# Optimization experiments

Measured on AMD Instinct MI355X. Metric: run time of the kernel, lower is better.

The kernel has to match this reference:

```python
import jax, jax.numpy as jnp
import numpy as np

EPS = 1e-8      # covariance regularizer (module-level `eps` in source repo)
ALPHA = 0.8     # style/content blend (module-level `alpha` in source repo)
SV_THRESH = 1e-5  # singular-value cutoff from the source


def _flatten(x):
    # x: [1, H, W, C] -> [C, H*W]
    xt = jnp.transpose(x[0], (2, 0, 1))  # C, H, W
    C = xt.shape[0]
    return xt.reshape(C, -1)


def _cov(f):
    # f: [C, N] already centered -> [C, C]
    C, N = f.shape
    return f @ f.T / (jnp.float32(N) - 1.0) + EPS * jnp.eye(C, dtype=f.dtype)


def _masked_pow(S, p):
    # Faithful to truncating columns with S <= 1e-5: zero their diag weight.
    mask = S > SV_THRESH
    S_safe = jnp.where(mask, S, 1.0)
    return jnp.where(mask, S_safe ** p, 0.0)


def setup_inputs() -> dict:
    key = jax.random.key(0)
    k1, k2 = jax.random.split(key)
    content = jax.random.normal(k1, (1, 128, 128, 512), dtype=jnp.float32)
    style = jax.random.normal(k2, (1, 128, 128, 512), dtype=jnp.float32)
    return {"content": content, "style": style}


def reference(content, style):
    H, W, C = content.shape[1], content.shape[2], content.shape[3]

    content_flat = _flatten(content)  # [C, Hc*Wc]
    style_flat = _flatten(style)      # [C, Hs*Ws]

    mc = content_flat.mean(axis=1, keepdims=True)
    fc = content_flat - mc
    ms = style_flat.mean(axis=1, keepdims=True)
    fs = style_flat - ms

    fcfc = _cov(fc)
    fsfs = _cov(fs)

    # tf.svd on a symmetric PSD matrix: S descending, U orthonormal.
    Uc, Sc, _ = jnp.linalg.svd(fcfc)
    Us, Ss, _ = jnp.linalg.svd(fsfs)

    # Whitening: Uc diag(Sc^-1/2) Uc^T (truncated cols == zeroed diag entries)
    Dc = _masked_pow(Sc, -0.5)
    whiten = (Uc * Dc[None, :]) @ Uc.T  # [C, C]
    fc_hat = whiten @ fc                # [C, N]

    # Coloring: Us diag(Ss^1/2) Us^T
    Ds = _masked_pow(Ss, 0.5)
    color = (Us * Ds[None, :]) @ Us.T
    fcs_hat = color @ fc_hat + ms

    blended = ALPHA * fcs_hat + (1.0 - ALPHA) * (fc + mc)  # [C, N]
    blended = blended.reshape(C, H, W)
    return jnp.transpose(blended, (1, 2, 0))[None]  # [1, H, W, C]
```

## Files before the change

### kernel.cpp

```cpp
#include <hip/hip_runtime.h>
#include <math.h>

#define NPIX 16384
#define CCH  512
#define MS   262144

typedef unsigned short u16;
typedef unsigned int u32;
typedef __attribute__((ext_vector_type(8))) short bf16x8;
typedef __attribute__((ext_vector_type(4))) float f32x4;

__device__ __forceinline__ u16 f2bf(float f) {
  u32 u = __builtin_bit_cast(u32, f);
  u += 0x7fffu + ((u >> 16) & 1u);
  return (u16)(u >> 16);
}
__device__ __forceinline__ float b2f(u16 h) {
  u32 u = ((u32)h) << 16;
  return __builtin_bit_cast(float, u);
}

typedef const __attribute__((address_space(1))) u32* gp_t;
typedef __attribute__((address_space(3))) u32* lp_t;
__device__ __forceinline__ void gl_lds16(const void* g, void* l) {
  __builtin_amdgcn_global_load_lds((gp_t)g, (lp_t)l, 16, 0, 0);
}

__device__ __forceinline__ void stage4(const u16* tile, size_t stride, int rl,
                                       int k0, u16* lds, int lane) {
  int lr = lane >> 4;
  int cg = (lane & 15) ^ ((rl + lr) & 15);
  gl_lds16(tile + (size_t)(rl + lr) * stride + k0 + cg * 8,
           lds + (size_t)rl * 128);
}
__device__ __forceinline__ bf16x8 fragld(const u16* lds, int row, int cl) {
  return *(const bf16x8*)&lds[(size_t)row * 128 + (size_t)((cl ^ (row & 15)) << 3)];
}

__device__ __forceinline__ void stage8_64(const u16* tile, size_t stride, int rl,
                                          int k0, u16* lds, int lane) {
  int lr = lane >> 3;
  int cg = (lane & 7) ^ ((rl + lr) & 7);
  gl_lds16(tile + (size_t)(rl + lr) * stride + k0 + cg * 8,
           lds + (size_t)rl * 64);
}
__device__ __forceinline__ bf16x8 fragld64(const u16* lds, int row, int cl) {
  return *(const bf16x8*)&lds[(size_t)row * 64 + (size_t)((cl ^ (row & 7)) << 3)];
}

__global__ __launch_bounds__(256) void prep_k(const float* __restrict__ Xc,
                                              const float* __restrict__ Xs,
                                              float* __restrict__ sums,
                                              u16* __restrict__ fct,
                                              u16* __restrict__ fcb) {
  int b = blockIdx.z;
  const float* X = b ? Xs : Xc;
  u16* outT = fct + (size_t)b * ((size_t)CCH * NPIX);
  __shared__ float T[64][65];
  __shared__ float red2[64][4];
  int n0 = blockIdx.x * 64, c0 = blockIdx.y * 64;
  int t = threadIdx.x;
  int cr = t & 15, nr = t >> 4;
  #pragma unroll
  for (int rr = 0; rr < 4; ++rr) {
    int n = nr + rr * 16;
    float4 v = *(const float4*)&X[(size_t)(n0 + n) * CCH + c0 + cr * 4];
    T[n][cr * 4 + 0] = v.x;
    T[n][cr * 4 + 1] = v.y;
    T[n][cr * 4 + 2] = v.z;
    T[n][cr * 4 + 3] = v.w;
    if (b == 0) {
      ushort4 q;
      q.x = f2bf(v.x); q.y = f2bf(v.y); q.z = f2bf(v.z); q.w = f2bf(v.w);
      *(ushort4*)&fcb[(size_t)(n0 + n) * CCH + c0 + cr * 4] = q;
    }
  }
  __syncthreads();
  int cl = t >> 2, np = (t & 3) * 16;
  size_t obase = (size_t)(c0 + cl) * NPIX + n0 + np;
  float s = 0.f;
  #pragma unroll
  for (int i = 0; i < 16; i += 4) {
    float v0 = T[np + i + 0][cl], v1 = T[np + i + 1][cl];
    float v2 = T[np + i + 2][cl], v3 = T[np + i + 3][cl];
    s += v0 + v1 + v2 + v3;
    ushort4 o;
    o.x = f2bf(v0); o.y = f2bf(v1); o.z = f2bf(v2); o.w = f2bf(v3);
    *(ushort4*)&outT[obase + i] = o;
  }
  red2[cl][t & 3] = s;
  __syncthreads();
  if (t < 64) {
    float cs = red2[t][0] + red2[t][1] + red2[t][2] + red2[t][3];
    atomicAdd(&sums[b * CCH + c0 + t], cs);
  }
}

__global__ __launch_bounds__(256, 4) void gram_mfma(const u16* __restrict__ fct,
                                                    float* __restrict__ G) {
  int kc = blockIdx.x;
  int pair = blockIdx.y;
  int b = blockIdx.z;
  int bi = pair >> 2, bj = pair & 3;
  const u16* Xb = fct + (size_t)b * ((size_t)CCH * NPIX);
  float* Gb = G + (size_t)b * MS;
  __shared__ u16 As[128 * 64];
  __shared__ u16 Bs[128 * 64];
  int tid = threadIdx.x, w = tid >> 6, lane = tid & 63;
  int qm = w & 1, qn = w >> 1;
  const u16* ssrc = (w < 2) ? Xb + (size_t)(bi * 128) * NPIX
                            : Xb + (size_t)(bj * 128) * NPIX;
  u16* sdst = (w < 2) ? As : Bs;
  int rbase = (w & 1) * 64;
  f32x4 acc[4][4];
  #pragma unroll
  for (int t = 0; t < 4; ++t)
    #pragma unroll
    for (int u = 0; u < 4; ++u) acc[t][u] = (f32x4)(0.f);

  for (int st = 0; st < 8; ++st) {
    int k0 = kc * 512 + st * 64;
    __syncthreads();
    #pragma unroll
    for (int i = 0; i < 8; ++i) stage8_64(ssrc, NPIX, rbase + i * 8, k0, sdst, lane);
    __syncthreads();
    #pragma unroll
    for (int s = 0; s < 2; ++s) {
      int cl = s * 4 + (lane >> 4);
      bf16x8 a[4], bb[4];
      #pragma unroll
      for (int t = 0; t < 4; ++t) a[t] = fragld64(As, qm * 64 + t * 16 + (lane & 15), cl);
      #pragma unroll
      for (int u = 0; u < 4; ++u) bb[u] = fragld64(Bs, qn * 64 + u * 16 + (lane & 15), cl);
      #pragma unroll
      for (int t = 0; t < 4; ++t)
        #pragma unroll
        for (int u = 0; u < 4; ++u)
          acc[t][u] = __builtin_amdgcn_mfma_f32_16x16x32_bf16(a[t], bb[u], acc[t][u], 0, 0, 0);
    }
  }
  #pragma unroll
  for (int t = 0; t < 4; ++t) {
    int row0 = bi * 128 + qm * 64 + t * 16 + (lane >> 4) * 4;
    #pragma unroll
    for (int u = 0; u < 4; ++u) {
      int col = bj * 128 + qn * 64 + u * 16 + (lane & 15);
      #pragma unroll
      for (int r4 = 0; r4 < 4; ++r4)
        atomicAdd(&Gb[(size_t)(row0 + r4) * CCH + col], acc[t][u][r4]);
    }
  }
}

__global__ __launch_bounds__(256) void cov_k(const float* __restrict__ G,
                                             const float* __restrict__ sums,
                                             float* __restrict__ cov,
                                             float* __restrict__ rowsum) {
  int idx = blockIdx.x * 256 + threadIdx.x;
  int b = idx >> 18;
  int ij = idx & (MS - 1);
  int i = ij >> 9, j = ij & 511;
  const float* s = sums + b * CCH;
  float v = (G[idx] - s[i] * s[j] * (1.f / (float)NPIX)) * (1.f / (float)(NPIX - 1));
  if (i == j) v += 1e-8f;
  cov[idx] = v;
  __shared__ float red[256];
  int t = threadIdx.x;
  red[t] = fabsf(v);
  __syncthreads();
  for (int st = 128; st > 0; st >>= 1) {
    if (t < st) red[t] += red[t + st];
    __syncthreads();
  }
  if (t == 0) atomicAdd(&rowsum[b * CCH + i], red[0]);
}

__global__ __launch_bounds__(256) void nsinit_k(const float* __restrict__ cov,
                                                const float* __restrict__ rowsum,
                                                float* __restrict__ snorm,
                                                float* __restrict__ coef,
                                                u16* __restrict__ Anh,
                                                u16* __restrict__ Anl,
                                                u16* __restrict__ Z0) {
  __shared__ float red[256];
  int tid = threadIdx.x, blk = blockIdx.x;
  float m = fmaxf(rowsum[tid], rowsum[tid + 256]);
  red[tid] = m; __syncthreads();
  for (int s = 128; s > 0; s >>= 1) {
    if (tid < s) red[tid] = fmaxf(red[tid], red[tid + s]);
    __syncthreads();
  }
  float snc = red[0]; __syncthreads();
  m = fmaxf(rowsum[512 + tid], rowsum[768 + tid]);
  red[tid] = m; __syncthreads();
  for (int s = 128; s > 0; s >>= 1) {
    if (tid < s) red[tid] = fmaxf(red[tid], red[tid + s]);
    __syncthreads();
  }
  float sns = red[0];
  if (blk == 0 && tid == 0) {
    snorm[0] = snc; snorm[1] = sns;
    coef[0] = 0.8f * sqrtf(sns / snc);
  }
  int idx = blk * 256 + tid;
  int b = idx >> 18;
  int ij = idx & (MS - 1);
  int diag = (ij >> 9) == (ij & 511);
  float av = cov[idx] * (b ? 1.f / sns : 1.f / snc);
  u16 hi = f2bf(av);
  Anh[idx] = hi;
  Anl[idx] = f2bf(av - b2f(hi));
  float t0 = (diag ? 3.f - av : -av) * 0.70710678f;
  Z0[idx] = f2bf(t0);
}

struct MM16 {
  const u16* A[4];
  const u16* B[4];
  void* D[4];
  float scale, diag;
  int outFp32;
};

__global__ __launch_bounds__(256) void mm16_k(MM16 args) {
  int z = blockIdx.z;
  const u16* __restrict__ A = args.A[z];
  const u16* __restrict__ B = args.B[z];
  int bi = blockIdx.y, bj = blockIdx.x;
  __shared__ u16 As[64 * 128];
  __shared__ u16 Bs[64 * 128];
  int tid = threadIdx.x, w = tid >> 6, lane = tid & 63;
  int qm = w & 1, qn = w >> 1;
  const u16* ssrc = ((w < 2) ? A + (size_t)(bi * 64) * CCH : B + (size_t)(bj * 64) * CCH);
  u16* sdst = (w < 2) ? As : Bs;
  int rbase = (w & 1) * 32;
  f32x4 acc[2][2];
  #pragma unroll
  for (int t = 0; t < 2; ++t)
    #pragma unroll
    for (int u = 0; u < 2; ++u) acc[t][u] = (f32x4)(0.f);

  for (int st = 0; st < 4; ++st) {
    int k0 = st * 128;
    __syncthreads();
    #pragma unroll
    for (int i = 0; i < 8; ++i) stage4(ssrc, CCH, rbase + i * 4, k0, sdst, lane);
    __syncthreads();
    #pragma unroll
    for (int s = 0; s < 4; ++s) {
      int cl = s * 4 + (lane >> 4);
      bf16x8 a[2], bb[2];
      #pragma unroll
      for (int t = 0; t < 2; ++t) a[t] = fragld(As, qm * 32 + t * 16 + (lane & 15), cl);
      #pragma unroll
      for (int u = 0; u < 2; ++u) bb[u] = fragld(Bs, qn * 32 + u * 16 + (lane & 15), cl);
      #pragma unroll
      for (int t = 0; t < 2; ++t)
        #pragma unroll
        for (int u = 0; u < 2; ++u)
          acc[t][u] = __builtin_amdgcn_mfma_f32_16x16x32_bf16(a[t], bb[u], acc[t][u], 0, 0, 0);
    }
  }
  float sc = args.scale;
  #pragma unroll
  for (int t = 0; t < 2; ++t) {
    int row0 = bi * 64 + qm * 32 + t * 16 + (lane >> 4) * 4;
    #pragma unroll
    for (int u = 0; u < 2; ++u) {
      int col = bj * 64 + qn * 32 + u * 16 + (lane & 15);
      #pragma unroll
      for (int r4 = 0; r4 < 4; ++r4) {
        float v = sc * acc[t][u][r4];
        if (row0 + r4 == col) v += args.diag;
        size_t o = (size_t)(row0 + r4) * CCH + col;
        if (args.outFp32) ((float*)args.D[z])[o] = v;
        else ((u16*)args.D[z])[o] = f2bf(v);
      }
    }
  }
}

__global__ __launch_bounds__(256) void symsplit_k(const float* __restrict__ src,
                                                  u16* __restrict__ hi,
                                                  u16* __restrict__ lo) {
  int b = blockIdx.y;
  int ij = blockIdx.x * 256 + threadIdx.x;
  int i = ij >> 9, j = ij & 511;
  size_t base = (size_t)b * MS;
  float v = 0.5f * (src[base + ij] + src[base + (size_t)j * CCH + i]);
  u16 h = f2bf(v);
  hi[base + ij] = h;
  lo[base + ij] = f2bf(v - b2f(h));
}

struct MMS {
  const u16 *Ah[4], *Al[4], *Bh[4], *Bl[4];
  const u16 *Eh[4], *El[4];
  u16 *Dh[4], *Dl[4];
  float *D32[4];
  u16 *Db[4];
  float scale, beta;
  const float* coefPtr;
};

__global__ __launch_bounds__(256) void mmsplit_k(MMS args) {
  int z = blockIdx.z;
  int bi = blockIdx.y, bj = blockIdx.x;
  __shared__ u16 Ash[64 * 128], Asl[64 * 128], Bsh[64 * 128], Bsl[64 * 128];
  int tid = threadIdx.x, w = tid >> 6, lane = tid & 63;
  int qm = w & 1, qn = w >> 1;
  const u16* sp = (w == 0) ? args.Ah[z] : (w == 1) ? args.Al[z]
                : (w == 2) ? args.Bh[z] : args.Bl[z];
  const u16* ssrc = sp + (size_t)(((w < 2) ? bi : bj) * 64) * CCH;
  u16* sdst = (w == 0) ? Ash : (w == 1) ? Asl : (w == 2) ? Bsh : Bsl;
  f32x4 acc[2][2];
  #pragma unroll
  for (int t = 0; t < 2; ++t)
    #pragma unroll
    for (int u = 0; u < 2; ++u) acc[t][u] = (f32x4)(0.f);

  for (int st = 0; st < 4; ++st) {
    int k0 = st * 128;
    __syncthreads();
    #pragma unroll
    for (int i = 0; i < 16; ++i) stage4(ssrc, CCH, i * 4, k0, sdst, lane);
    __syncthreads();
    #pragma unroll
    for (int s = 0; s < 4; ++s) {
      int cl = s * 4 + (lane >> 4);
      bf16x8 ah[2], al[2], bh[2], bl[2];
      #pragma unroll
      for (int t = 0; t < 2; ++t) {
        int row = qm * 32 + t * 16 + (lane & 15);
        ah[t] = fragld(Ash, row, cl);
        al[t] = fragld(Asl, row, cl);
      }
      #pragma unroll
      for (int u = 0; u < 2; ++u) {
        int row = qn * 32 + u * 16 + (lane & 15);
        bh[u] = fragld(Bsh, row, cl);
        bl[u] = fragld(Bsl, row, cl);
      }
      #pragma unroll
      for (int t = 0; t < 2; ++t)
        #pragma unroll
        for (int u = 0; u < 2; ++u) {
          acc[t][u] = __builtin_amdgcn_mfma_f32_16x16x32_bf16(ah[t], bh[u], acc[t][u], 0, 0, 0);
          acc[t][u] = __builtin_amdgcn_mfma_f32_16x16x32_bf16(ah[t], bl[u], acc[t][u], 0, 0, 0);
          acc[t][u] = __builtin_amdgcn_mfma_f32_16x16x32_bf16(al[t], bh[u], acc[t][u], 0, 0, 0);
        }
    }
  }
  float sc = args.scale;
  if (args.coefPtr) sc *= *args.coefPtr;
  #pragma unroll
  for (int t = 0; t < 2; ++t) {
    int row0 = bi * 64 + qm * 32 + t * 16 + (lane >> 4) * 4;
    #pragma unroll
    for (int u = 0; u < 2; ++u) {
      int col = bj * 64 + qn * 32 + u * 16 + (lane & 15);
      #pragma unroll
      for (int r4 = 0; r4 < 4; ++r4) {
        size_t o = (size_t)(row0 + r4) * CCH + col;
        float v = sc * acc[t][u][r4];
        if (args.beta != 0.f) v += args.beta * (b2f(args.Eh[z][o]) + b2f(args.El[z][o]));
        if (args.D32[z]) args.D32[z][o] = v;
        if (args.Dh[z]) {
          u16 h = f2bf(v);
          args.Dh[z][o] = h;
          args.Dl[z][o] = f2bf(v - b2f(h));
        }
        if (args.Db[z]) args.Db[z][o] = f2bf(v);
      }
    }
  }
}

__global__ __launch_bounds__(256) void mconst_k(const u16* __restrict__ Mb,
                                                const float* __restrict__ sums,
                                                float* __restrict__ mconst) {
  int c = blockIdx.x * 8 + (threadIdx.x >> 5);
  int l = threadIdx.x & 31;
  float s = 0.f;
  #pragma unroll
  for (int k = 0; k < 16; ++k) {
    int j = l + 32 * k;
    s += b2f(Mb[(size_t)c * CCH + j]) * sums[j];
  }
  s += __shfl_down(s, 16, 32);
  s += __shfl_down(s, 8, 32);
  s += __shfl_down(s, 4, 32);
  s += __shfl_down(s, 2, 32);
  s += __shfl_down(s, 1, 32);
  if (l == 0) mconst[c] = (0.8f * sums[512 + c] - s) * (1.f / (float)NPIX);
}

__global__ __launch_bounds__(256) void apply_mfma(const u16* __restrict__ fcb,
                                                  const u16* __restrict__ Mb,
                                                  const float* __restrict__ mconst,
                                                  const float* __restrict__ X,
                                                  float* __restrict__ out) {
  int bi = blockIdx.y;
  int bj = blockIdx.x;
  __shared__ u16 As[128 * 128];
  __shared__ u16 Bs[128 * 128];
  int tid = threadIdx.x, w = tid >> 6, lane = tid & 63;
  int qm = w & 1, qn = w >> 1;
  const u16* ssrc = (w < 2) ? fcb + (size_t)(bi * 128) * CCH
                            : Mb + (size_t)(bj * 128) * CCH;
  u16* sdst = (w < 2) ? As : Bs;
  int rbase = (w & 1) * 64;
  f32x4 acc[4][4];
  #pragma unroll
  for (int t = 0; t < 4; ++t)
    #pragma unroll
    for (int u = 0; u < 4; ++u) acc[t][u] = (f32x4)(0.f);

  for (int st = 0; st < 4; ++st) {
    int k0 = st * 128;
    __syncthreads();
    #pragma unroll
    for (int i = 0; i < 16; ++i) stage4(ssrc, CCH, rbase + i * 4, k0, sdst, lane);
    __syncthreads();
    #pragma unroll
    for (int s = 0; s < 4; ++s) {
      int cl = s * 4 + (lane >> 4);
      bf16x8 a[4], bb[4];
      #pragma unroll
      for (int t = 0; t < 4; ++t) a[t] = fragld(As, qm * 64 + t * 16 + (lane & 15), cl);
      #pragma unroll
      for (int u = 0; u < 4; ++u) bb[u] = fragld(Bs, qn * 64 + u * 16 + (lane & 15), cl);
      #pragma unroll
      for (int t = 0; t < 4; ++t)
        #pragma unroll
        for (int u = 0; u < 4; ++u)
          acc[t][u] = __builtin_amdgcn_mfma_f32_16x16x32_bf16(a[t], bb[u], acc[t][u], 0, 0, 0);
    }
  }
  #pragma unroll
  for (int t = 0; t < 4; ++t) {
    int row0 = bi * 128 + qm * 64 + t * 16 + (lane >> 4) * 4;
    #pragma unroll
    for (int u = 0; u < 4; ++u) {
      int col = bj * 128 + qn * 64 + u * 16 + (lane & 15);
      float cst = mconst[col];
      #pragma unroll
      for (int r4 = 0; r4 < 4; ++r4) {
        size_t o = (size_t)(row0 + r4) * CCH + col;
        out[o] = acc[t][u][r4] + cst + 0.2f * X[o];
      }
    }
  }
}

extern "C" void kernel_launch(void* const* d_in, const int* in_sizes, int n_in,
                              void* d_out, int out_size, void* d_ws, size_t ws_size,
                              hipStream_t stream) {
  const float* Xc = (const float*)d_in[0];
  const float* Xs = (const float*)d_in[1];
  float* out = (float*)d_out;

  float* f = (float*)d_ws;
  float* sums   = f;
  float* rowsum = f + 1024;
  float* G      = f + 2048;
  float* cov    = G + 2 * MS;
  float* snorm  = cov + 2 * MS;
  float* coef   = snorm + 8;
  float* mconst = coef + 8;
  float* Zf     = mconst + 512;

  u16* h   = (u16*)(Zf + 2 * MS);
  u16* fct = h;
  u16* fcb = h + (size_t)2 * CCH * NPIX;
  const size_t B2 = 2 * MS;
  u16* Anh  = fct + 0 * B2;
  u16* Anl  = fct + 1 * B2;
  u16* Y1   = fct + 2 * B2;
  u16* Ya   = fct + 3 * B2;
  u16* Z0   = fct + 4 * B2;
  u16* Z1   = fct + 5 * B2;
  u16* Tb   = fct + 6 * B2;
  u16* Zfsh = fct + 7 * B2;
  u16* Zfsl = fct + 8 * B2;
  u16* Ph   = fct + 9 * B2;
  u16* Pl   = fct + 10 * B2;
  u16* Qh   = fct + 11 * B2;
  u16* Ql   = fct + 12 * B2;
  u16* Zrsh = fct + 13 * B2;
  u16* Zrsl = fct + 14 * B2;
  u16* W2h  = fct + 15 * B2;
  u16* W2l  = W2h + MS;
  u16* Mb   = W2l + MS;

  hipMemsetAsync(d_ws, 0, (2048 + 2 * MS) * sizeof(float), stream);

  prep_k<<<dim3(256, 8, 2), 256, 0, stream>>>(Xc, Xs, sums, fct, fcb);
  gram_mfma<<<dim3(32, 16, 2), 256, 0, stream>>>(fct, G);
  cov_k<<<2048, 256, 0, stream>>>(G, sums, cov, rowsum);
  nsinit_k<<<2048, 256, 0, stream>>>(cov, rowsum, snorm, coef, Anh, Anl, Z0);

  {
    MM16 y1{};
    y1.A[0] = Anh;      y1.B[0] = Z0;      y1.D[0] = Y1;
    y1.A[1] = Anh + MS; y1.B[1] = Z0 + MS; y1.D[1] = Y1 + MS;
    y1.scale = 1.f; y1.diag = 0.f; y1.outFp32 = 0;
    mm16_k<<<dim3(8, 8, 2), 256, 0, stream>>>(y1);
  }
  {
    MM16 t{};
    t.A[0] = Z0;      t.B[0] = Y1;      t.D[0] = Tb;
    t.A[1] = Z0 + MS; t.B[1] = Y1 + MS; t.D[1] = Tb + MS;
    t.scale = -1.f; t.diag = 3.f; t.outFp32 = 0;
    mm16_k<<<dim3(8, 8, 2), 256, 0, stream>>>(t);
  }
  {
    MM16 yz{};
    yz.A[0] = Y1;      yz.B[0] = Tb;      yz.D[0] = Ya;
    yz.A[1] = Y1 + MS; yz.B[1] = Tb + MS; yz.D[1] = Ya + MS;
    yz.A[2] = Tb;      yz.B[2] = Z0;      yz.D[2] = Z1;
    yz.A[3] = Tb + MS; yz.B[3] = Z0 + MS; yz.D[3] = Z1 + MS;
    yz.scale = 0.5f; yz.diag = 0.f; yz.outFp32 = 0;
    mm16_k<<<dim3(8, 8, 4), 256, 0, stream>>>(yz);
  }
  {
    MM16 t{};
    t.A[0] = Z1;      t.B[0] = Ya;      t.D[0] = Tb;
    t.A[1] = Z1 + MS; t.B[1] = Ya + MS; t.D[1] = Tb + MS;
    t.scale = -1.f; t.diag = 3.f; t.outFp32 = 0;
    mm16_k<<<dim3(8, 8, 2), 256, 0, stream>>>(t);
  }
  {
    MM16 yz{};
    yz.A[0] = Ya;      yz.B[0] = Tb;      yz.D[0] = Y1;
    yz.A[1] = Ya + MS; yz.B[1] = Tb + MS; yz.D[1] = Y1 + MS;
    yz.A[2] = Tb;      yz.B[2] = Z1;      yz.D[2] = Z0;
    yz.A[3] = Tb + MS; yz.B[3] = Z1 + MS; yz.D[3] = Z0 + MS;
    yz.scale = 0.5f; yz.diag = 0.f; yz.outFp32 = 0;
    mm16_k<<<dim3(8, 8, 4), 256, 0, stream>>>(yz);
  }
  {
    MM16 t{};
    t.A[0] = Z0;      t.B[0] = Y1;      t.D[0] = Tb;
    t.A[1] = Z0 + MS; t.B[1] = Y1 + MS; t.D[1] = Tb + MS;
    t.scale = -1.f; t.diag = 3.f; t.outFp32 = 0;
    mm16_k<<<dim3(8, 8, 2), 256, 0, stream>>>(t);
  }
  {
    MM16 zf{};
    zf.A[0] = Tb;      zf.B[0] = Z0;      zf.D[0] = Zf;
    zf.A[1] = Tb + MS; zf.B[1] = Z0 + MS; zf.D[1] = Zf + MS;
    zf.scale = 0.5f; zf.diag = 0.f; zf.outFp32 = 1;
    mm16_k<<<dim3(8, 8, 2), 256, 0, stream>>>(zf);
  }

  symsplit_k<<<dim3(1024, 2), 256, 0, stream>>>(Zf, Zfsh, Zfsl);

  MMS pq{};
  for (int b = 0; b < 2; ++b) {
    pq.Ah[b] = Zfsh + b * MS; pq.Al[b] = Zfsl + b * MS;
    pq.Bh[b] = Anh + b * MS;  pq.Bl[b] = Anl + b * MS;
    pq.Dh[b] = Ph + b * MS;   pq.Dl[b] = Pl + b * MS;
    pq.Ah[2 + b] = Zfsh + b * MS; pq.Al[2 + b] = Zfsl + b * MS;
    pq.Bh[2 + b] = Zfsh + b * MS; pq.Bl[2 + b] = Zfsl + b * MS;
    pq.Dh[2 + b] = Qh + b * MS;   pq.Dl[2 + b] = Ql + b * MS;
  }
  pq.scale = 1.f;
  mmsplit_k<<<dim3(8, 8, 4), 256, 0, stream>>>(pq);

  MMS zr{};
  for (int b = 0; b < 2; ++b) {
    zr.Ah[b] = Ph + b * MS;   zr.Al[b] = Pl + b * MS;
    zr.Bh[b] = Qh + b * MS;   zr.Bl[b] = Ql + b * MS;
    zr.Eh[b] = Zfsh + b * MS; zr.El[b] = Zfsl + b * MS;
    zr.D32[b] = Zf + b * MS;
  }
  zr.scale = -0.5f; zr.beta = 1.5f;
  mmsplit_k<<<dim3(8, 8, 2), 256, 0, stream>>>(zr);

  symsplit_k<<<dim3(1024, 2), 256, 0, stream>>>(Zf, Zrsh, Zrsl);

  MMS wv{};
  wv.Ah[0] = Anh + MS;  wv.Al[0] = Anl + MS;
  wv.Bh[0] = Zrsh + MS; wv.Bl[0] = Zrsl + MS;
  wv.Dh[0] = W2h; wv.Dl[0] = W2l;
  wv.scale = 1.f;
  mmsplit_k<<<dim3(8, 8, 1), 256, 0, stream>>>(wv);

  MMS mv{};
  mv.Ah[0] = W2h;  mv.Al[0] = W2l;
  mv.Bh[0] = Zrsh; mv.Bl[0] = Zrsl;
  mv.Db[0] = Mb;
  mv.scale = 1.f; mv.coefPtr = coef;
  mmsplit_k<<<dim3(8, 8, 1), 256, 0, stream>>>(mv);

  mconst_k<<<64, 256, 0, stream>>>(Mb, sums, mconst);
  apply_mfma<<<dim3(4, 128), 256, 0, stream>>>(fcb, Mb, mconst, Xc, out);
}
```

Measured before the change: 319.9 us.

## Replace atomic Gram accumulation with split-K partial buffers and a reduction pass

Each Gram block now handles twice as many K steps and writes its 128x128 partial tile with plain stores into a scratch area, reusing the output buffer, instead of issuing float atomics into a shared G. The covariance kernel sums the 16 partials per element before normalizing. This removes the global atomic contention and most of the large workspace memset. The cost is extra partial-buffer traffic, 16 reads per element in the reduce, and half as many Gram blocks in flight.

Result: faster. 279.9 us (-12.5%).

```diff
diff --git a/kernel.cpp b/kernel.cpp
--- a/kernel.cpp
+++ b/kernel.cpp
@@ -96,14 +96,13 @@
   }
 }
 
-__global__ __launch_bounds__(256, 4) void gram_mfma(const u16* __restrict__ fct,
-                                                    float* __restrict__ G) {
+__global__ __launch_bounds__(256, 4) void gram_part(const u16* __restrict__ fct,
+                                                    float* __restrict__ Gp) {
   int kc = blockIdx.x;
   int pair = blockIdx.y;
   int b = blockIdx.z;
   int bi = pair >> 2, bj = pair & 3;
   const u16* Xb = fct + (size_t)b * ((size_t)CCH * NPIX);
-  float* Gb = G + (size_t)b * MS;
   __shared__ u16 As[128 * 64];
   __shared__ u16 Bs[128 * 64];
   int tid = threadIdx.x, w = tid >> 6, lane = tid & 63;
@@ -118,8 +117,8 @@
     #pragma unroll
     for (int u = 0; u < 4; ++u) acc[t][u] = (f32x4)(0.f);
 
-  for (int st = 0; st < 8; ++st) {
-    int k0 = kc * 512 + st * 64;
+  for (int st = 0; st < 16; ++st) {
+    int k0 = kc * 1024 + st * 64;
     __syncthreads();
     #pragma unroll
     for (int i = 0; i < 8; ++i) stage8_64(ssrc, NPIX, rbase + i * 8, k0, sdst, lane);
@@ -139,29 +138,37 @@
           acc[t][u] = __builtin_amdgcn_mfma_f32_16x16x32_bf16(a[t], bb[u], acc[t][u], 0, 0, 0);
     }
   }
+  size_t tbase = ((size_t)(b * 16 + kc) * 16 + pair) * 16384;
   #pragma unroll
   for (int t = 0; t < 4; ++t) {
-    int row0 = bi * 128 + qm * 64 + t * 16 + (lane >> 4) * 4;
+    int row0 = qm * 64 + t * 16 + (lane >> 4) * 4;
     #pragma unroll
     for (int u = 0; u < 4; ++u) {
-      int col = bj * 128 + qn * 64 + u * 16 + (lane & 15);
+      int col = qn * 64 + u * 16 + (lane & 15);
       #pragma unroll
       for (int r4 = 0; r4 < 4; ++r4)
-        atomicAdd(&Gb[(size_t)(row0 + r4) * CCH + col], acc[t][u][r4]);
-    }
-  }
-}
-
-__global__ __launch_bounds__(256) void cov_k(const float* __restrict__ G,
-                                             const float* __restrict__ sums,
-                                             float* __restrict__ cov,
-                                             float* __restrict__ rowsum) {
+        Gp[tbase + (size_t)(row0 + r4) * 128 + col] = acc[t][u][r4];
+    }
+  }
+}
+
+__global__ __launch_bounds__(256) void gram_reduce(const float* __restrict__ Gp,
+                                                   const float* __restrict__ sums,
+                                                   float* __restrict__ cov,
+                                                   float* __restrict__ rowsum) {
   int idx = blockIdx.x * 256 + threadIdx.x;
   int b = idx >> 18;
   int ij = idx & (MS - 1);
   int i = ij >> 9, j = ij & 511;
+  int pair = ((i >> 7) << 2) | (j >> 7);
+  int lij = ((i & 127) << 7) | (j & 127);
+  size_t base = ((size_t)(b * 16) * 16 + pair) * 16384 + lij;
+  float g = 0.f;
+  #pragma unroll
+  for (int kc = 0; kc < 16; ++kc)
+    g += Gp[base + (size_t)kc * (16 * 16384)];
   const float* s = sums + b * CCH;
-  float v = (G[idx] - s[i] * s[j] * (1.f / (float)NPIX)) * (1.f / (float)(NPIX - 1));
+  float v = (g - s[i] * s[j] * (1.f / (float)NPIX)) * (1.f / (float)(NPIX - 1));
   if (i == j) v += 1e-8f;
   cov[idx] = v;
   __shared__ float red[256];
@@ -463,12 +470,13 @@
   float* f = (float*)d_ws;
   float* sums   = f;
   float* rowsum = f + 1024;
-  float* G      = f + 2048;
-  float* cov    = G + 2 * MS;
+  float* cov    = f + 2048 + 2 * MS;
   float* snorm  = cov + 2 * MS;
   float* coef   = snorm + 8;
   float* mconst = coef + 8;
   float* Zf     = mconst + 512;
+
+  float* Gp = (float*)d_out;
 
   u16* h   = (u16*)(Zf + 2 * MS);
   u16* fct = h;
@@ -493,11 +501,11 @@
   u16* W2l  = W2h + MS;
   u16* Mb   = W2l + MS;
 
-  hipMemsetAsync(d_ws, 0, (2048 + 2 * MS) * sizeof(float), stream);
+  hipMemsetAsync(d_ws, 0, 2048 * sizeof(float), stream);
 
   prep_k<<<dim3(256, 8, 2), 256, 0, stream>>>(Xc, Xs, sums, fct, fcb);
-  gram_mfma<<<dim3(32, 16, 2), 256, 0, stream>>>(fct, G);
-  cov_k<<<2048, 256, 0, stream>>>(G, sums, cov, rowsum);
+  gram_part<<<dim3(16, 16, 2), 256, 0, stream>>>(fct, Gp);
+  gram_reduce<<<2048, 256, 0, stream>>>(Gp, sums, cov, rowsum);
   nsinit_k<<<2048, 256, 0, stream>>>(cov, rowsum, snorm, coef, Anh, Anl, Z0);
 
   {
```
